# Kernel tuning notes

Measured on AMD Instinct MI355X. Metric: run time of the kernel, lower is better.

The kernel has to match this reference:

```python
import jax, jax.numpy as jnp
import numpy as np

B, T, HIDDEN, QLR = 1, 2560, 7168, 1536
N_HEADS, HEAD_DIM, ROPE_DIM, TOPK = 64, 128, 64, 2048
LN_EPS = 1e-6


def _rope(x, cos, sin):
    # non-interleaved (half-split) rotary: pairs are (x[i], x[i+d/2])
    d = x.shape[-1] // 2
    x1, x2 = x[..., :d], x[..., d:]
    return jnp.concatenate([x1 * cos - x2 * sin, x1 * sin + x2 * cos], axis=-1)


def setup_inputs() -> dict:
    key = jax.random.key(0)
    ks = jax.random.split(key, 6)
    x = jax.random.normal(ks[0], (B, T, HIDDEN), dtype=jnp.float32)
    qr = jax.random.normal(ks[1], (B, T, QLR), dtype=jnp.float32)
    # rope tables (theta = 10000)
    inv_freq = 1.0 / (10000.0 ** (jnp.arange(0, ROPE_DIM, 2, dtype=jnp.float32) / ROPE_DIM))
    angles = jnp.arange(T, dtype=jnp.float32)[:, None] * inv_freq[None, :]  # [T, 32]
    freqs_cos = jnp.cos(angles)
    freqs_sin = jnp.sin(angles)
    # causal additive mask
    i = jnp.arange(T)
    mask = jnp.where(i[None, :, None] >= i[None, None, :], 0.0, -1e9).astype(jnp.float32)  # [1,T,T]
    # params (torch Linear stored transposed so y = x @ W)
    s = 0.02
    wq_b = jax.random.normal(ks[2], (QLR, N_HEADS * HEAD_DIM), dtype=jnp.float32) * s
    wk_w = jax.random.normal(ks[3], (HIDDEN, HEAD_DIM), dtype=jnp.float32) * s
    k_gamma = jnp.ones((HEAD_DIM,), dtype=jnp.float32)
    k_beta = jnp.zeros((HEAD_DIM,), dtype=jnp.float32)
    wproj = jax.random.normal(ks[4], (HIDDEN, N_HEADS), dtype=jnp.float32) * s
    return {"x": x, "qr": qr, "freqs_cos": freqs_cos, "freqs_sin": freqs_sin,
            "mask": mask, "wq_b": wq_b, "wk_w": wk_w, "k_gamma": k_gamma,
            "k_beta": k_beta, "wproj": wproj}


def reference(x, qr, freqs_cos, freqs_sin, mask, wq_b, wk_w, k_gamma, k_beta, wproj):
    bsz, seqlen, _ = x.shape
    # queries
    q = (qr @ wq_b).reshape(bsz, seqlen, N_HEADS, HEAD_DIM)
    q_pe, q_nope = q[..., :ROPE_DIM], q[..., ROPE_DIM:]
    q_pe = _rope(q_pe, freqs_cos[None, :, None, :], freqs_sin[None, :, None, :])
    q = jnp.concatenate([q_pe, q_nope], axis=-1)  # [B,T,H,D]
    # keys: layernorm(wk(x))
    k = x @ wk_w  # [B,T,D]
    mu = jnp.mean(k, axis=-1, keepdims=True)
    var = jnp.mean(jnp.square(k - mu), axis=-1, keepdims=True)
    k = (k - mu) / jnp.sqrt(var + LN_EPS) * k_gamma + k_beta
    k_pe, k_nope = k[..., :ROPE_DIM], k[..., ROPE_DIM:]
    k_pe = _rope(k_pe, freqs_cos[None, :, :], freqs_sin[None, :, :])
    k = jnp.concatenate([k_pe, k_nope], axis=-1)  # [B,S,D]
    # per-head weights
    weights = (x @ wproj) * (N_HEADS ** -0.5) * (HEAD_DIM ** -0.5)  # [B,T,H]
    # relu score + weighted head reduce
    logits = jax.nn.relu(jnp.einsum('bthd,bsd->btsh', q, k))  # [B,T,S,H]
    index_score = jnp.einsum('btsh,bth->bts', logits, weights) + mask
    # top-k + scatter mask
    kk = min(TOPK, seqlen)
    _, topk_idx = jax.lax.top_k(index_score, kk)  # [B,T,K]
    index_mask = jnp.full((bsz, seqlen, seqlen), -1e9, dtype=jnp.float32)
    bi = jnp.arange(bsz)[:, None, None]
    ti = jnp.arange(seqlen)[None, :, None]
    index_mask = index_mask.at[bi, ti, topk_idx].set(0.0)
    return index_mask
```

## Files before the change

### kernel.cpp

```cpp
#include <hip/hip_runtime.h>
#include <cstdint>

#define T_SEQ   2560
#define HID     7168
#define QLRD    1536
#define NHEAD   64
#define HDIM    128
#define TOPK    2048
#define T0SEL   2048
#define NSEL    512

#define QHOFF 0
#define QLOFF 2097152
#define KOFF  4194304
#define WOFF  4521984
#define KHOFF 4554752
#define KLOFF 4718592
#define SOFF  5242880

typedef _Float16 half8 __attribute__((ext_vector_type(8)));
typedef _Float16 half4v __attribute__((ext_vector_type(4)));
typedef float    floatx16 __attribute__((ext_vector_type(16)));

__device__ __forceinline__ void lds_barrier() {
    asm volatile("s_waitcnt lgkmcnt(0)" ::: "memory");
    __builtin_amdgcn_s_barrier();
}

#define SWZ(row) ((((row) >> 3) & 3) << 3)

__global__ __launch_bounds__(384) void kw_kernel(
        const float* __restrict__ x, const float* __restrict__ wk,
        const float* __restrict__ wp, float* __restrict__ Pk,
        float* __restrict__ Pw, long pkstride, long pwstride, int klen) {
    const int t0 = blockIdx.x * 64;
    const int chunk = blockIdx.y;
    const int k0 = chunk * klen;
    const int kl = min(klen, HID - k0);
    const int steps = kl >> 5;
    float* pk = Pk + (size_t)chunk * pkstride;
    float* pw = Pw + (size_t)chunk * pwstride;

    const int tid = threadIdx.x;
    const int lane = tid & 63;
    const int wv = tid >> 6;
    const int wt = wv / 3;
    const int wn2 = wv % 3;
    const int l31 = lane & 31;
    const int kb = (lane >> 5) * 8;

    __shared__ __align__(16) _Float16 Ah0[64 * 40], Al0[64 * 40];
    __shared__ __align__(16) _Float16 Bh0[192 * 40], Bl0[192 * 40];
    __shared__ __align__(16) _Float16 Ah1[64 * 40], Al1[64 * 40];
    __shared__ __align__(16) _Float16 Bh1[192 * 40], Bl1[192 * 40];

    const int am = tid >> 2;
    const int ak = (tid & 3) * 8;
    const int akS = ak ^ SWZ(am);
    const int bkr = (tid / 48) * 4;
    const int bnr = (tid % 48) * 4;

    const float* aB = x + (size_t)(t0 + am) * HID + k0 + ak;
    const float* bsrc; int bld, bcol;
    if (bnr < 128) { bsrc = wk; bld = 128; bcol = bnr; }
    else           { bsrc = wp; bld = 64;  bcol = bnr - 128; }
    const float* bB = bsrc + (size_t)(k0 + bkr) * bld + bcol;

    float4 pa0, pa1, pb0, pb1, pb2, pb3;

#define KWLOAD(KK) do {                                                        \
    const float* ap_ = aB + (size_t)(KK) * 32;                                 \
    const float* bp_ = bB + (size_t)(KK) * 32 * bld;                           \
    if (tid < 256) { pa0 = *(const float4*)(ap_ + 0);                          \
                     pa1 = *(const float4*)(ap_ + 4); }                        \
    pb0 = *(const float4*)(bp_ + 0 * (size_t)bld);                             \
    pb1 = *(const float4*)(bp_ + 1 * (size_t)bld);                             \
    pb2 = *(const float4*)(bp_ + 2 * (size_t)bld);                             \
    pb3 = *(const float4*)(bp_ + 3 * (size_t)bld);                             \
} while (0)

#define KWCONVERT(AH, AL, BH, BL) do {                                         \
    if (tid < 256) {                                                           \
        float av[8];                                                           \
        *(float4*)&av[0] = pa0; *(float4*)&av[4] = pa1;                        \
        half8 ha, la;                                                          \
        _Pragma("unroll")                                                      \
        for (int i = 0; i < 8; ++i) {                                          \
            float v = av[i];                                                   \
            _Float16 hi = (_Float16)v;                                         \
            ha[i] = hi;                                                        \
            la[i] = (_Float16)(v - (float)hi);                                 \
        }                                                                      \
        *(half8*)&AH[am * 40 + akS] = ha;                                      \
        *(half8*)&AL[am * 40 + akS] = la;                                      \
    }                                                                          \
    {                                                                          \
        float bv[4][4];                                                        \
        *(float4*)&bv[0][0] = pb0; *(float4*)&bv[1][0] = pb1;                  \
        *(float4*)&bv[2][0] = pb2; *(float4*)&bv[3][0] = pb3;                  \
        _Pragma("unroll")                                                      \
        for (int j = 0; j < 4; ++j) {                                          \
            const int bkS = bkr ^ SWZ(bnr + j);                                \
            half4v hb, lb;                                                     \
            _Pragma("unroll")                                                  \
            for (int i = 0; i < 4; ++i) {                                      \
                float v = bv[i][j] * 64.0f;                                    \
                _Float16 hi = (_Float16)v;                                     \
                hb[i] = hi;                                                    \
                lb[i] = (_Float16)(v - (float)hi);                             \
            }                                                                  \
            *(half4v*)&BH[(bnr + j) * 40 + bkS] = hb;                          \
            *(half4v*)&BL[(bnr + j) * 40 + bkS] = lb;                          \
        }                                                                      \
    }                                                                          \
} while (0)

    const int rowA  = wt * 32 + l31;
    const int xA    = SWZ(rowA);
    const int rowB0 = wn2 * 64 + l31;
    const int xB0   = SWZ(rowB0);
    const int rowB1 = rowB0 + 32;
    const int xB1   = SWZ(rowB1);

#define KWMFMA(AH, AL, BH, BL) do {                                            \
    __builtin_amdgcn_s_setprio(1);                                             \
    _Pragma("unroll")                                                          \
    for (int c = 0; c < 2; ++c) {                                              \
        const int ka = c * 16 + kb;                                            \
        half8 ah  = *(const half8*)&AH[rowA * 40 + (ka ^ xA)];                 \
        half8 al  = *(const half8*)&AL[rowA * 40 + (ka ^ xA)];                 \
        half8 bh0 = *(const half8*)&BH[rowB0 * 40 + (ka ^ xB0)];               \
        half8 bl0 = *(const half8*)&BL[rowB0 * 40 + (ka ^ xB0)];               \
        half8 bh1 = *(const half8*)&BH[rowB1 * 40 + (ka ^ xB1)];               \
        half8 bl1 = *(const half8*)&BL[rowB1 * 40 + (ka ^ xB1)];               \
        Chh0 = __builtin_amdgcn_mfma_f32_32x32x16_f16(ah, bh0, Chh0, 0, 0, 0); \
        Chl0 = __builtin_amdgcn_mfma_f32_32x32x16_f16(ah, bl0, Chl0, 0, 0, 0); \
        Clh0 = __builtin_amdgcn_mfma_f32_32x32x16_f16(al, bh0, Clh0, 0, 0, 0); \
        Chh1 = __builtin_amdgcn_mfma_f32_32x32x16_f16(ah, bh1, Chh1, 0, 0, 0); \
        Chl1 = __builtin_amdgcn_mfma_f32_32x32x16_f16(ah, bl1, Chl1, 0, 0, 0); \
        Clh1 = __builtin_amdgcn_mfma_f32_32x32x16_f16(al, bh1, Clh1, 0, 0, 0); \
    }                                                                          \
    __builtin_amdgcn_s_setprio(0);                                             \
} while (0)

    floatx16 Z = {0.f,0.f,0.f,0.f,0.f,0.f,0.f,0.f,0.f,0.f,0.f,0.f,0.f,0.f,0.f,0.f};
    floatx16 Chh0 = Z, Chl0 = Z, Clh0 = Z;
    floatx16 Chh1 = Z, Chl1 = Z, Clh1 = Z;

    KWLOAD(0);
    KWCONVERT(Ah0, Al0, Bh0, Bl0);
    KWLOAD(1);
    __builtin_amdgcn_sched_barrier(0);
    lds_barrier();

    for (int ks = 0; ks < steps; ks += 2) {
        KWMFMA(Ah0, Al0, Bh0, Bl0);
        KWCONVERT(Ah1, Al1, Bh1, Bl1);
        KWLOAD(min(ks + 2, steps - 1));
        __builtin_amdgcn_sched_barrier(0);
        lds_barrier();
        KWMFMA(Ah1, Al1, Bh1, Bl1);
        KWCONVERT(Ah0, Al0, Bh0, Bl0);
        KWLOAD(min(ks + 3, steps - 1));
        __builtin_amdgcn_sched_barrier(0);
        lds_barrier();
    }
#undef KWLOAD
#undef KWCONVERT
#undef KWMFMA

    const int rbase = wt * 32 + 4 * (lane >> 5);
#pragma unroll
    for (int r = 0; r < 16; ++r) {
        int trow = t0 + rbase + (r & 3) + 8 * (r >> 2);
        float v0 = ((Chh0[r] + Chl0[r]) + Clh0[r]) * 0.015625f;
        float v1 = ((Chh1[r] + Chl1[r]) + Clh1[r]) * 0.015625f;
        int c0 = wn2 * 64 + l31;
        if (wn2 < 2) {
            pk[(size_t)trow * 128 + c0] = v0;
            pk[(size_t)trow * 128 + c0 + 32] = v1;
        } else if (trow >= T0SEL) {
            pw[(size_t)(trow - T0SEL) * 64 + c0 - 128] = v0;
            pw[(size_t)(trow - T0SEL) * 64 + c0 - 96] = v1;
        }
    }
}

__global__ void reduce2_kernel(float* __restrict__ dk, const float* __restrict__ sk,
                               long kstr, float* __restrict__ dw,
                               const float* __restrict__ sw, long wstr, int nchunk) {
    int i = blockIdx.x * 256 + threadIdx.x;
    if (i < 327680) {
        float s = sk[i];
        for (int c = 1; c < nchunk; ++c) s += sk[(size_t)c * kstr + i];
        dk[i] = s;
    } else {
        int j = i - 327680;
        float s = sw[j];
        for (int c = 1; c < nchunk; ++c) s += sw[(size_t)c * wstr + j];
        dw[j] = s;
    }
}

__global__ void lnrope_kernel(const float* __restrict__ fcos, const float* __restrict__ fsin,
                              const float* __restrict__ gamma, const float* __restrict__ beta,
                              const float* __restrict__ Kbuf, float* __restrict__ Wbuf,
                              _Float16* __restrict__ KhG, _Float16* __restrict__ KlG) {
#pragma clang fp contract(off)
    const int s = blockIdx.x;
    const int d = threadIdx.x;
    __shared__ float red[128];
    __shared__ float kn[128];
    float kv = Kbuf[(size_t)s * 128 + d];
    red[d] = kv;
    __syncthreads();
    for (int off = 64; off > 0; off >>= 1) {
        if (d < off) red[d] += red[d + off];
        __syncthreads();
    }
    float mu = red[0] / 128.0f;
    __syncthreads();
    float dv = kv - mu;
    red[d] = dv * dv;
    __syncthreads();
    for (int off = 64; off > 0; off >>= 1) {
        if (d < off) red[d] += red[d + off];
        __syncthreads();
    }
    float var = red[0] / 128.0f;
    float nrm = dv / sqrtf(var + 1e-6f);
    nrm = nrm * gamma[d] + beta[d];
    kn[d] = nrm;
    __syncthreads();
    float o;
    if (d < 64) {
        int p = d & 31;
        float c = fcos[s * 32 + p], sn = fsin[s * 32 + p];
        if (d < 32) o = kn[d] * c - kn[d + 32] * sn;
        else        o = kn[d - 32] * sn + kn[d] * c;
    } else {
        o = kn[d];
    }
    _Float16 hi = (_Float16)o;
    _Float16 lo = (_Float16)(o - (float)hi);
    KhG[(size_t)s * 128 + d] = hi;
    KlG[(size_t)s * 128 + d] = lo;
    if (s >= T0SEL && d < 64) {
        Wbuf[(size_t)(s - T0SEL) * 64 + d] *= (0.125f * 0.08838834764831845f);
    }
}

__global__ __launch_bounds__(256, 2) void q_kernel(
        const float* __restrict__ qr, const float* __restrict__ wqb,
        const float* __restrict__ fcos, const float* __restrict__ fsin,
        _Float16* __restrict__ QhG, _Float16* __restrict__ QlG) {
    const int head = blockIdx.x;
    const int bx = blockIdx.y;
    const int tid = threadIdx.x;
    const int lane = tid & 63;
    const int wv = tid >> 6;
    const int wt = wv >> 1, wn = wv & 1;
    const int l31 = lane & 31;
    const int kb = (lane >> 5) * 8;

    __shared__ __align__(16) _Float16 Ah0[64 * 40], Al0[64 * 40];
    __shared__ __align__(16) _Float16 Bh0[128 * 40], Bl0[128 * 40];
    __shared__ __align__(16) _Float16 Ah1[64 * 40], Al1[64 * 40];
    __shared__ __align__(16) _Float16 Bh1[128 * 40], Bl1[128 * 40];

    const int am = tid >> 2;
    const int ak = (tid & 3) * 8;
    const int akS = ak ^ SWZ(am);
    const int bn = (tid & 31) * 4;
    const int bk = (tid >> 5) * 4;

    const float* aB = qr + (size_t)(T0SEL + bx * 64 + am) * QLRD + ak;
    const float* bB = wqb + (size_t)bk * 8192 + head * 128 + bn;

    float4 pa0, pa1, pb0, pb1, pb2, pb3;

#define QLOAD(KK) do {                                                         \
    const float* ap_ = aB + (size_t)(KK) * 32;                                 \
    const float* bp_ = bB + (size_t)(KK) * 32 * 8192;                          \
    pa0 = *(const float4*)(ap_ + 0);                                           \
    pa1 = *(const float4*)(ap_ + 4);                                           \
    pb0 = *(const float4*)(bp_ + 0 * 8192);                                    \
    pb1 = *(const float4*)(bp_ + 1 * 8192);                                    \
    pb2 = *(const float4*)(bp_ + 2 * 8192);                                    \
    pb3 = *(const float4*)(bp_ + 3 * 8192);                                    \
} while (0)

#define QCONVERT(AH, AL, BH, BL) do {                                          \
    float av[8];                                                               \
    *(float4*)&av[0] = pa0; *(float4*)&av[4] = pa1;                            \
    half8 ha, la;                                                              \
    _Pragma("unroll")                                                          \
    for (int i = 0; i < 8; ++i) {                                              \
        float v = av[i];                                                       \
        _Float16 hi = (_Float16)v;                                             \
        ha[i] = hi;                                                            \
        la[i] = (_Float16)(v - (float)hi);                                     \
    }                                                                          \
    *(half8*)&AH[am * 40 + akS] = ha;                                          \
    *(half8*)&AL[am * 40 + akS] = la;                                          \
    float bv[4][4];                                                            \
    *(float4*)&bv[0][0] = pb0; *(float4*)&bv[1][0] = pb1;                      \
    *(float4*)&bv[2][0] = pb2; *(float4*)&bv[3][0] = pb3;                      \
    _Pragma("unroll")                                                          \
    for (int j = 0; j < 4; ++j) {                                              \
        const int bkS = bk ^ SWZ(bn + j);                                      \
        half4v hb, lb;                                                         \
        _Pragma("unroll")                                                      \
        for (int i = 0; i < 4; ++i) {                                          \
            float v = bv[i][j] * 64.0f;                                        \
            _Float16 hi = (_Float16)v;                                         \
            hb[i] = hi;                                                        \
            lb[i] = (_Float16)(v - (float)hi);                                 \
        }                                                                      \
        *(half4v*)&BH[(bn + j) * 40 + bkS] = hb;                               \
        *(half4v*)&BL[(bn + j) * 40 + bkS] = lb;                               \
    }                                                                          \
} while (0)

    const int rowA  = wt * 32 + l31;
    const int xA    = SWZ(rowA);
    const int rowB0 = wn * 64 + l31;
    const int xB0   = SWZ(rowB0);
    const int rowB1 = rowB0 + 32;
    const int xB1   = SWZ(rowB1);

#define QMFMA(AH, AL, BH, BL) do {                                             \
    __builtin_amdgcn_s_setprio(1);                                             \
    _Pragma("unroll")                                                          \
    for (int c = 0; c < 2; ++c) {                                              \
        const int ka = c * 16 + kb;                                            \
        half8 ah  = *(const half8*)&AH[rowA * 40 + (ka ^ xA)];                 \
        half8 al  = *(const half8*)&AL[rowA * 40 + (ka ^ xA)];                 \
        half8 bh0 = *(const half8*)&BH[rowB0 * 40 + (ka ^ xB0)];               \
        half8 bl0 = *(const half8*)&BL[rowB0 * 40 + (ka ^ xB0)];               \
        half8 bh1 = *(const half8*)&BH[rowB1 * 40 + (ka ^ xB1)];               \
        half8 bl1 = *(const half8*)&BL[rowB1 * 40 + (ka ^ xB1)];               \
        Chh0 = __builtin_amdgcn_mfma_f32_32x32x16_f16(ah, bh0, Chh0, 0, 0, 0); \
        Chl0 = __builtin_amdgcn_mfma_f32_32x32x16_f16(ah, bl0, Chl0, 0, 0, 0); \
        Clh0 = __builtin_amdgcn_mfma_f32_32x32x16_f16(al, bh0, Clh0, 0, 0, 0); \
        Chh1 = __builtin_amdgcn_mfma_f32_32x32x16_f16(ah, bh1, Chh1, 0, 0, 0); \
        Chl1 = __builtin_amdgcn_mfma_f32_32x32x16_f16(ah, bl1, Chl1, 0, 0, 0); \
        Clh1 = __builtin_amdgcn_mfma_f32_32x32x16_f16(al, bh1, Clh1, 0, 0, 0); \
    }                                                                          \
    __builtin_amdgcn_s_setprio(0);                                             \
} while (0)

    floatx16 Z = {0.f,0.f,0.f,0.f,0.f,0.f,0.f,0.f,0.f,0.f,0.f,0.f,0.f,0.f,0.f,0.f};
    floatx16 Chh0 = Z, Chl0 = Z, Clh0 = Z;
    floatx16 Chh1 = Z, Chl1 = Z, Clh1 = Z;

    const int steps = QLRD / 32;

    QLOAD(0);
    QCONVERT(Ah0, Al0, Bh0, Bl0);
    QLOAD(1);
    __builtin_amdgcn_sched_barrier(0);
    lds_barrier();

    for (int ks = 0; ks < steps; ks += 2) {
        QMFMA(Ah0, Al0, Bh0, Bl0);
        QCONVERT(Ah1, Al1, Bh1, Bl1);
        QLOAD(min(ks + 2, steps - 1));
        __builtin_amdgcn_sched_barrier(0);
        lds_barrier();
        QMFMA(Ah1, Al1, Bh1, Bl1);
        QCONVERT(Ah0, Al0, Bh0, Bl0);
        QLOAD(min(ks + 3, steps - 1));
        __builtin_amdgcn_sched_barrier(0);
        lds_barrier();
    }
#undef QLOAD
#undef QCONVERT
#undef QMFMA

    {
#pragma clang fp contract(off)
        const int tbase = bx * 64 + wt * 32 + 4 * (lane >> 5);
#pragma unroll
        for (int r = 0; r < 16; ++r) {
            int tl = tbase + (r & 3) + 8 * (r >> 2);
            float v0 = ((Chh0[r] + Chl0[r]) + Clh0[r]) * 0.015625f;
            float v1 = ((Chh1[r] + Chl1[r]) + Clh1[r]) * 0.015625f;
            float o0, o1;
            if (wn == 0) {
                int tg = T0SEL + tl;
                float c = fcos[tg * 32 + l31];
                float s = fsin[tg * 32 + l31];
                o0 = v0 * c - v1 * s;
                o1 = v0 * s + v1 * c;
            } else {
                o0 = v0; o1 = v1;
            }
            int d0 = wn * 64 + l31;
            size_t off = (size_t)head * 65536 + (size_t)tl * 128;
            _Float16 h0 = (_Float16)o0;
            _Float16 h1 = (_Float16)o1;
            QhG[off + d0] = h0;
            QlG[off + d0] = (_Float16)(o0 - (float)h0);
            QhG[off + d0 + 32] = h1;
            QlG[off + d0 + 32] = (_Float16)(o1 - (float)h1);
        }
    }
}

__global__ __launch_bounds__(256) void score_kernel(
        const _Float16* __restrict__ Qh, const _Float16* __restrict__ Ql,
        const _Float16* __restrict__ Kh, const _Float16* __restrict__ Kl,
        const float* __restrict__ Wbuf, float* __restrict__ S0,
        float* __restrict__ S1, int hcnt) {
    const int bid = blockIdx.x;
    const int tt0 = (bid & 15) * 32;
    const int s0  = (bid >> 4) * 128;
    const int hb  = blockIdx.y * hcnt;
    float* __restrict__ dst = blockIdx.y ? S1 : S0;
    const int tid = threadIdx.x;
    const int wv  = tid >> 6;
    const int lane = tid & 63;
    const int l31 = lane & 31;
    const int kb  = (lane >> 5) * 8;

    __shared__ __align__(16) _Float16 AhA[32 * 136];
    __shared__ __align__(16) _Float16 AlA[32 * 136];
    __shared__ __align__(16) _Float16 AhB[32 * 136];
    __shared__ __align__(16) _Float16 AlB[32 * 136];
    __shared__ float WsT[64 * 36];

    half8 Bh[8], Bl[8];
    {
        const int srow = s0 + wv * 32 + l31;
        const _Float16* kh = Kh + (size_t)srow * 128 + kb;
        const _Float16* kl = Kl + (size_t)srow * 128 + kb;
#pragma unroll
        for (int c = 0; c < 8; ++c) {
            Bh[c] = *(const half8*)(kh + c * 16);
            Bl[c] = *(const half8*)(kl + c * 16);
        }
    }
#pragma unroll
    for (int r = 0; r < 8; ++r) {
        int idx = tid + 256 * r;
        int row = idx >> 6, h = idx & 63;
        WsT[h * 36 + row] = Wbuf[(size_t)(tt0 + row) * 64 + h];
    }

    const int srow0 = tid >> 4;
    const int scc0  = (tid & 15) * 8;
    const int srow1 = srow0 + 16;
    const int scc1  = scc0;

    const _Float16* qhp = Qh + (size_t)hb * 65536 + (size_t)tt0 * 128;
    const _Float16* qlp = Ql + (size_t)hb * 65536 + (size_t)tt0 * 128;

    half8 sh0 = *(const half8*)&qhp[srow0 * 128 + scc0];
    half8 sh1 = *(const half8*)&qhp[srow1 * 128 + scc1];
    half8 sl0 = *(const half8*)&qlp[srow0 * 128 + scc0];
    half8 sl1 = *(const half8*)&qlp[srow1 * 128 + scc1];
    *(half8*)&AhA[srow0 * 136 + scc0] = sh0;
    *(half8*)&AhA[srow1 * 136 + scc1] = sh1;
    *(half8*)&AlA[srow0 * 136 + scc0] = sl0;
    *(half8*)&AlA[srow1 * 136 + scc1] = sl1;
    qhp += 65536; qlp += 65536;
    sh0 = *(const half8*)&qhp[srow0 * 128 + scc0];
    sh1 = *(const half8*)&qhp[srow1 * 128 + scc1];
    sl0 = *(const half8*)&qlp[srow0 * 128 + scc0];
    sl1 = *(const half8*)&qlp[srow1 * 128 + scc1];
    __builtin_amdgcn_sched_barrier(0);
    lds_barrier();

    float S[16];
#pragma unroll
    for (int r = 0; r < 16; ++r) S[r] = 0.0f;

#define SCORE_COMPUTE(AH, AL, HIDX)                                            \
    {                                                                          \
        floatx16 C0 = {0.f,0.f,0.f,0.f,0.f,0.f,0.f,0.f,                        \
                       0.f,0.f,0.f,0.f,0.f,0.f,0.f,0.f};                       \
        floatx16 C2 = C0, C3 = C0;                                             \
        __builtin_amdgcn_s_setprio(1);                                         \
        _Pragma("unroll")                                                      \
        for (int c = 0; c < 8; ++c) {                                          \
            half8 a_h = *(const half8*)&AH[l31 * 136 + c * 16 + kb];           \
            half8 a_l = *(const half8*)&AL[l31 * 136 + c * 16 + kb];           \
            C0 = __builtin_amdgcn_mfma_f32_32x32x16_f16(a_h, Bh[c], C0, 0, 0, 0); \
            C2 = __builtin_amdgcn_mfma_f32_32x32x16_f16(a_h, Bl[c], C2, 0, 0, 0); \
            C3 = __builtin_amdgcn_mfma_f32_32x32x16_f16(a_l, Bh[c], C3, 0, 0, 0); \
        }                                                                      \
        __builtin_amdgcn_s_setprio(0);                                         \
        const float* wb = &WsT[(HIDX) * 36 + 4 * (lane >> 5)];                 \
        float4 w0 = *(const float4*)(wb + 0);                                  \
        float4 w1 = *(const float4*)(wb + 8);                                  \
        float4 w2 = *(const float4*)(wb + 16);                                 \
        float4 w3 = *(const float4*)(wb + 24);                                 \
        float w[16] = {w0.x, w0.y, w0.z, w0.w, w1.x, w1.y, w1.z, w1.w,         \
                       w2.x, w2.y, w2.z, w2.w, w3.x, w3.y, w3.z, w3.w};        \
        _Pragma("unroll")                                                      \
        for (int r = 0; r < 16; ++r) {                                         \
            float L = (C0[r] + C2[r]) + C3[r];                                 \
            S[r] += w[r] * fmaxf(L, 0.0f);                                     \
        }                                                                      \
    }

    for (int h = 0; h < hcnt; h += 2) {
        SCORE_COMPUTE(AhA, AlA, hb + h)
        *(half8*)&AhB[srow0 * 136 + scc0] = sh0;
        *(half8*)&AhB[srow1 * 136 + scc1] = sh1;
        *(half8*)&AlB[srow0 * 136 + scc0] = sl0;
        *(half8*)&AlB[srow1 * 136 + scc1] = sl1;
        qhp += 65536; qlp += 65536;
        sh0 = *(const half8*)&qhp[srow0 * 128 + scc0];
        sh1 = *(const half8*)&qhp[srow1 * 128 + scc1];
        sl0 = *(const half8*)&qlp[srow0 * 128 + scc0];
        sl1 = *(const half8*)&qlp[srow1 * 128 + scc1];
        __builtin_amdgcn_sched_barrier(0);
        lds_barrier();

        SCORE_COMPUTE(AhB, AlB, hb + h + 1)
        *(half8*)&AhA[srow0 * 136 + scc0] = sh0;
        *(half8*)&AhA[srow1 * 136 + scc1] = sh1;
        *(half8*)&AlA[srow0 * 136 + scc0] = sl0;
        *(half8*)&AlA[srow1 * 136 + scc1] = sl1;
        qhp += 65536; qlp += 65536;
        sh0 = *(const half8*)&qhp[srow0 * 128 + scc0];
        sh1 = *(const half8*)&qhp[srow1 * 128 + scc1];
        sl0 = *(const half8*)&qlp[srow0 * 128 + scc0];
        sl1 = *(const half8*)&qlp[srow1 * 128 + scc1];
        __builtin_amdgcn_sched_barrier(0);
        lds_barrier();
    }
#undef SCORE_COMPUTE

    const int scol = s0 + wv * 32 + l31;
#pragma unroll
    for (int r = 0; r < 16; ++r) {
        int trow = tt0 + (r & 3) + 8 * (r >> 2) + 4 * (lane >> 5);
        dst[(size_t)trow * 2560 + scol] = S[r] + 0.0f;
    }
}

__global__ void finalize_kernel(float* __restrict__ out, const float* __restrict__ S1) {
    const int row_id = blockIdx.x;
    const int tid = threadIdx.x;

    if (row_id < T0SEL) {
        const float4 zero4 = make_float4(0.0f, 0.0f, 0.0f, 0.0f);
        const float4 neg4 = make_float4(-1000000000.0f, -1000000000.0f,
                                        -1000000000.0f, -1000000000.0f);
        for (int i = tid; i < T_SEQ / 4; i += 256) {
            *(float4*)&out[(size_t)row_id * T_SEQ + i * 4] = (i * 4 < TOPK) ? zero4 : neg4;
        }
        return;
    }

    const int t = row_id;
    const int n = t + 1;
    float* row = out + (size_t)t * T_SEQ;
    const float* s1p = S1 ? (S1 + (size_t)(t - T0SEL) * T_SEQ) : nullptr;

    __shared__ unsigned U[T_SEQ];
    __shared__ int hist[256];
    __shared__ int aux[256];
    __shared__ unsigned sh_prefix;
    __shared__ int sh_kneed;

    for (int i = tid; i < T_SEQ; i += 256) {
        unsigned u = 0u;
        if (i < n) {
            float sc = row[i];
            if (s1p) sc += s1p[i];
            int b = __float_as_int(sc);
            u = (b < 0) ? ~((unsigned)b) : (((unsigned)b) | 0x80000000u);
        }
        U[i] = u;
    }
    if (tid == 0) { sh_prefix = 0u; sh_kneed = TOPK; }
    __syncthreads();

    for (int pass = 0; pass < 4; ++pass) {
        const int shift = 24 - 8 * pass;
        const unsigned himask = (pass == 0) ? 0u : (0xFFFFFFFFu << (shift + 8));
        hist[tid] = 0;
        __syncthreads();
        const unsigned pre = sh_prefix;
        const int kneed = sh_kneed;
        for (int i = tid; i < T_SEQ; i += 256) {
            unsigned u = U[i];
            if ((u & himask) == pre) atomicAdd(&hist[(u >> shift) & 255], 1);
        }
        __syncthreads();
        aux[tid] = hist[tid];
        __syncthreads();
        for (int off = 1; off < 256; off <<= 1) {
            int a = (tid + off < 256) ? aux[tid + off] : 0;
            __syncthreads();
            aux[tid] += a;
            __syncthreads();
        }
        int above = (tid < 255) ? aux[tid + 1] : 0;
        if (above < kneed && kneed <= aux[tid]) {
            sh_prefix = pre | (((unsigned)tid) << shift);
            sh_kneed = kneed - above;
        }
        __syncthreads();
    }
    const unsigned theta = sh_prefix;
    const int r = sh_kneed;

    const int s_lo = tid * 10, s_hi = s_lo + 10;
    int c = 0;
    for (int s = s_lo; s < s_hi; ++s) c += (U[s] == theta);
    aux[tid] = c;
    __syncthreads();
    for (int off = 1; off < 256; off <<= 1) {
        int a = (tid >= off) ? aux[tid - off] : 0;
        __syncthreads();
        aux[tid] += a;
        __syncthreads();
    }
    int rank = aux[tid] - c;
    for (int s = s_lo; s < s_hi; ++s) {
        unsigned u = U[s];
        bool sel = (u > theta) || (u == theta && rank < r);
        if (u == theta) ++rank;
        row[s] = sel ? 0.0f : -1000000000.0f;
    }
}

extern "C" void kernel_launch(void* const* d_in, const int* in_sizes, int n_in,
                              void* d_out, int out_size, void* d_ws, size_t ws_size,
                              hipStream_t stream) {
    (void)in_sizes; (void)n_in; (void)out_size;
    const float* x     = (const float*)d_in[0];
    const float* qr    = (const float*)d_in[1];
    const float* fcos  = (const float*)d_in[2];
    const float* fsin  = (const float*)d_in[3];
    const float* wqb   = (const float*)d_in[5];
    const float* wk    = (const float*)d_in[6];
    const float* gamma = (const float*)d_in[7];
    const float* beta  = (const float*)d_in[8];
    const float* wp    = (const float*)d_in[9];

    float* out  = (float*)d_out;
    float* Kbuf = out + KOFF;
    float* Wbuf = out + WOFF;
    float* Sbuf = out + SOFF;
    _Float16* QhG = (_Float16*)(out + QHOFF);
    _Float16* QlG = (_Float16*)(out + QLOFF);
    _Float16* KhG = (_Float16*)(out + KHOFF);
    _Float16* KlG = (_Float16*)(out + KLOFF);

    const size_t need = (size_t)(6 * 327680 + 6 * 32768) * 4;
    int nchunk; int klen; float *Pk, *Pw; long pkstride, pwstride;
    if (ws_size >= need) {
        nchunk = 6; klen = 1216;
        Pk = (float*)d_ws;            pkstride = 327680;
        Pw = (float*)d_ws + 1966080;  pwstride = 32768;
    } else {
        nchunk = 2; klen = 3584;
        Pk = out + KOFF;  pkstride = 360448;
        Pw = out + WOFF;  pwstride = 360448;
    }

    const size_t s1_need = (size_t)NSEL * T_SEQ * sizeof(float);
    float* S1 = (ws_size >= s1_need) ? (float*)d_ws : nullptr;

    kw_kernel<<<dim3(40, nchunk), 384, 0, stream>>>(x, wk, wp, Pk, Pw, pkstride, pwstride, klen);
    reduce2_kernel<<<1408, 256, 0, stream>>>(Kbuf, Pk, pkstride, Wbuf, Pw, pwstride, nchunk);
    lnrope_kernel<<<T_SEQ, 128, 0, stream>>>(fcos, fsin, gamma, beta, Kbuf, Wbuf, KhG, KlG);
    q_kernel<<<dim3(64, 8), 256, 0, stream>>>(qr, wqb, fcos, fsin, QhG, QlG);
    if (S1) {
        score_kernel<<<dim3(320, 2), 256, 0, stream>>>(QhG, QlG, KhG, KlG, Wbuf, Sbuf, S1, 32);
    } else {
        score_kernel<<<dim3(320, 1), 256, 0, stream>>>(QhG, QlG, KhG, KlG, Wbuf, Sbuf, nullptr, 64);
    }
    finalize_kernel<<<T_SEQ, 256, 0, stream>>>(out, S1);
}
```

Before: 362.7 us.

## Process two heads per barrier stage and overlap epilogue with next MFMA

New measurement: 433.7 us. 19.6% more time.

```diff
diff --git a/kernel.cpp b/kernel.cpp
--- a/kernel.cpp
+++ b/kernel.cpp
@@ -408,7 +408,7 @@
     }
 }
 
-__global__ __launch_bounds__(256) void score_kernel(
+__global__ __launch_bounds__(256, 2) void score_kernel(
         const _Float16* __restrict__ Qh, const _Float16* __restrict__ Ql,
         const _Float16* __restrict__ Kh, const _Float16* __restrict__ Kl,
         const float* __restrict__ Wbuf, float* __restrict__ S0,
@@ -424,10 +424,10 @@
     const int l31 = lane & 31;
     const int kb  = (lane >> 5) * 8;
 
-    __shared__ __align__(16) _Float16 AhA[32 * 136];
-    __shared__ __align__(16) _Float16 AlA[32 * 136];
-    __shared__ __align__(16) _Float16 AhB[32 * 136];
-    __shared__ __align__(16) _Float16 AlB[32 * 136];
+    __shared__ __align__(16) _Float16 PhE[32 * 136], PlE[32 * 136];
+    __shared__ __align__(16) _Float16 PhO[32 * 136], PlO[32 * 136];
+    __shared__ __align__(16) _Float16 RhE[32 * 136], RlE[32 * 136];
+    __shared__ __align__(16) _Float16 RhO[32 * 136], RlO[32 * 136];
     __shared__ float WsT[64 * 36];
 
     half8 Bh[8], Bl[8];
@@ -451,24 +451,34 @@
     const int srow0 = tid >> 4;
     const int scc0  = (tid & 15) * 8;
     const int srow1 = srow0 + 16;
-    const int scc1  = scc0;
 
     const _Float16* qhp = Qh + (size_t)hb * 65536 + (size_t)tt0 * 128;
     const _Float16* qlp = Ql + (size_t)hb * 65536 + (size_t)tt0 * 128;
 
-    half8 sh0 = *(const half8*)&qhp[srow0 * 128 + scc0];
-    half8 sh1 = *(const half8*)&qhp[srow1 * 128 + scc1];
-    half8 sl0 = *(const half8*)&qlp[srow0 * 128 + scc0];
-    half8 sl1 = *(const half8*)&qlp[srow1 * 128 + scc1];
-    *(half8*)&AhA[srow0 * 136 + scc0] = sh0;
-    *(half8*)&AhA[srow1 * 136 + scc1] = sh1;
-    *(half8*)&AlA[srow0 * 136 + scc0] = sl0;
-    *(half8*)&AlA[srow1 * 136 + scc1] = sl1;
-    qhp += 65536; qlp += 65536;
-    sh0 = *(const half8*)&qhp[srow0 * 128 + scc0];
-    sh1 = *(const half8*)&qhp[srow1 * 128 + scc1];
-    sl0 = *(const half8*)&qlp[srow0 * 128 + scc0];
-    sl1 = *(const half8*)&qlp[srow1 * 128 + scc1];
+    half8 sEh0, sEh1, sEl0, sEl1;
+    half8 sOh0, sOh1, sOl0, sOl1;
+
+#define SLOAD(RH0, RH1, RL0, RL1) do {                                         \
+    RH0 = *(const half8*)&qhp[srow0 * 128 + scc0];                             \
+    RH1 = *(const half8*)&qhp[srow1 * 128 + scc0];                             \
+    RL0 = *(const half8*)&qlp[srow0 * 128 + scc0];                             \
+    RL1 = *(const half8*)&qlp[srow1 * 128 + scc0];                             \
+    qhp += 65536; qlp += 65536;                                                \
+} while (0)
+
+#define SWRITE(DH, DL, RH0, RH1, RL0, RL1) do {                                \
+    *(half8*)&DH[srow0 * 136 + scc0] = RH0;                                    \
+    *(half8*)&DH[srow1 * 136 + scc0] = RH1;                                    \
+    *(half8*)&DL[srow0 * 136 + scc0] = RL0;                                    \
+    *(half8*)&DL[srow1 * 136 + scc0] = RL1;                                    \
+} while (0)
+
+    SLOAD(sEh0, sEh1, sEl0, sEl1);
+    SWRITE(PhE, PlE, sEh0, sEh1, sEl0, sEl1);
+    SLOAD(sOh0, sOh1, sOl0, sOl1);
+    SWRITE(PhO, PlO, sOh0, sOh1, sOl0, sOl1);
+    SLOAD(sEh0, sEh1, sEl0, sEl1);
+    SLOAD(sOh0, sOh1, sOl0, sOl1);
     __builtin_amdgcn_sched_barrier(0);
     lds_barrier();
 
@@ -476,63 +486,70 @@
 #pragma unroll
     for (int r = 0; r < 16; ++r) S[r] = 0.0f;
 
-#define SCORE_COMPUTE(AH, AL, HIDX)                                            \
-    {                                                                          \
-        floatx16 C0 = {0.f,0.f,0.f,0.f,0.f,0.f,0.f,0.f,                        \
-                       0.f,0.f,0.f,0.f,0.f,0.f,0.f,0.f};                       \
-        floatx16 C2 = C0, C3 = C0;                                             \
-        __builtin_amdgcn_s_setprio(1);                                         \
-        _Pragma("unroll")                                                      \
-        for (int c = 0; c < 8; ++c) {                                          \
-            half8 a_h = *(const half8*)&AH[l31 * 136 + c * 16 + kb];           \
-            half8 a_l = *(const half8*)&AL[l31 * 136 + c * 16 + kb];           \
-            C0 = __builtin_amdgcn_mfma_f32_32x32x16_f16(a_h, Bh[c], C0, 0, 0, 0); \
-            C2 = __builtin_amdgcn_mfma_f32_32x32x16_f16(a_h, Bl[c], C2, 0, 0, 0); \
-            C3 = __builtin_amdgcn_mfma_f32_32x32x16_f16(a_l, Bh[c], C3, 0, 0, 0); \
-        }                                                                      \
-        __builtin_amdgcn_s_setprio(0);                                         \
-        const float* wb = &WsT[(HIDX) * 36 + 4 * (lane >> 5)];                 \
-        float4 w0 = *(const float4*)(wb + 0);                                  \
-        float4 w1 = *(const float4*)(wb + 8);                                  \
-        float4 w2 = *(const float4*)(wb + 16);                                 \
-        float4 w3 = *(const float4*)(wb + 24);                                 \
-        float w[16] = {w0.x, w0.y, w0.z, w0.w, w1.x, w1.y, w1.z, w1.w,         \
-                       w2.x, w2.y, w2.z, w2.w, w3.x, w3.y, w3.z, w3.w};        \
-        _Pragma("unroll")                                                      \
-        for (int r = 0; r < 16; ++r) {                                         \
-            float L = (C0[r] + C2[r]) + C3[r];                                 \
-            S[r] += w[r] * fmaxf(L, 0.0f);                                     \
-        }                                                                      \
-    }
-
-    for (int h = 0; h < hcnt; h += 2) {
-        SCORE_COMPUTE(AhA, AlA, hb + h)
-        *(half8*)&AhB[srow0 * 136 + scc0] = sh0;
-        *(half8*)&AhB[srow1 * 136 + scc1] = sh1;
-        *(half8*)&AlB[srow0 * 136 + scc0] = sl0;
-        *(half8*)&AlB[srow1 * 136 + scc1] = sl1;
-        qhp += 65536; qlp += 65536;
-        sh0 = *(const half8*)&qhp[srow0 * 128 + scc0];
-        sh1 = *(const half8*)&qhp[srow1 * 128 + scc1];
-        sl0 = *(const half8*)&qlp[srow0 * 128 + scc0];
-        sl1 = *(const half8*)&qlp[srow1 * 128 + scc1];
-        __builtin_amdgcn_sched_barrier(0);
-        lds_barrier();
-
-        SCORE_COMPUTE(AhB, AlB, hb + h + 1)
-        *(half8*)&AhA[srow0 * 136 + scc0] = sh0;
-        *(half8*)&AhA[srow1 * 136 + scc1] = sh1;
-        *(half8*)&AlA[srow0 * 136 + scc0] = sl0;
-        *(half8*)&AlA[srow1 * 136 + scc1] = sl1;
-        qhp += 65536; qlp += 65536;
-        sh0 = *(const half8*)&qhp[srow0 * 128 + scc0];
-        sh1 = *(const half8*)&qhp[srow1 * 128 + scc1];
-        sl0 = *(const half8*)&qlp[srow0 * 128 + scc0];
-        sl1 = *(const half8*)&qlp[srow1 * 128 + scc1];
-        __builtin_amdgcn_sched_barrier(0);
-        lds_barrier();
-    }
-#undef SCORE_COMPUTE
+#define SMFMA(AH, AL, CC0, CC2, CC3) do {                                      \
+    __builtin_amdgcn_s_setprio(1);                                             \
+    _Pragma("unroll")                                                          \
+    for (int c = 0; c < 8; ++c) {                                              \
+        half8 a_h = *(const half8*)&AH[l31 * 136 + c * 16 + kb];               \
+        half8 a_l = *(const half8*)&AL[l31 * 136 + c * 16 + kb];               \
+        CC0 = __builtin_amdgcn_mfma_f32_32x32x16_f16(a_h, Bh[c], CC0, 0, 0, 0);\
+        CC2 = __builtin_amdgcn_mfma_f32_32x32x16_f16(a_h, Bl[c], CC2, 0, 0, 0);\
+        CC3 = __builtin_amdgcn_mfma_f32_32x32x16_f16(a_l, Bh[c], CC3, 0, 0, 0);\
+    }                                                                          \
+    __builtin_amdgcn_s_setprio(0);                                             \
+} while (0)
+
+#define SEPI(CC0, CC2, CC3, HIDX) do {                                         \
+    const float* wb = &WsT[(HIDX) * 36 + 4 * (lane >> 5)];                     \
+    float4 w0 = *(const float4*)(wb + 0);                                      \
+    float4 w1 = *(const float4*)(wb + 8);                                      \
+    float4 w2 = *(const float4*)(wb + 16);                                     \
+    float4 w3 = *(const float4*)(wb + 24);                                     \
+    float w[16] = {w0.x, w0.y, w0.z, w0.w, w1.x, w1.y, w1.z, w1.w,             \
+                   w2.x, w2.y, w2.z, w2.w, w3.x, w3.y, w3.z, w3.w};            \
+    _Pragma("unroll")                                                          \
+    for (int r = 0; r < 16; ++r) {                                             \
+        float L = (CC0[r] + CC2[r]) + CC3[r];                                  \
+        S[r] += w[r] * fmaxf(L, 0.0f);                                         \
+    }                                                                          \
+} while (0)
+
+    const floatx16 Z = {0.f,0.f,0.f,0.f,0.f,0.f,0.f,0.f,0.f,0.f,0.f,0.f,0.f,0.f,0.f,0.f};
+
+    for (int p = 0; p < hcnt; p += 4) {
+        {
+            floatx16 C0e = Z, C2e = Z, C3e = Z;
+            floatx16 C0o = Z, C2o = Z, C3o = Z;
+            SMFMA(PhE, PlE, C0e, C2e, C3e);
+            SMFMA(PhO, PlO, C0o, C2o, C3o);
+            SWRITE(RhE, RlE, sEh0, sEh1, sEl0, sEl1);
+            SWRITE(RhO, RlO, sOh0, sOh1, sOl0, sOl1);
+            SLOAD(sEh0, sEh1, sEl0, sEl1);
+            SLOAD(sOh0, sOh1, sOl0, sOl1);
+            __builtin_amdgcn_sched_barrier(0);
+            lds_barrier();
+            SEPI(C0e, C2e, C3e, hb + p);
+            SEPI(C0o, C2o, C3o, hb + p + 1);
+        }
+        {
+            floatx16 C0e = Z, C2e = Z, C3e = Z;
+            floatx16 C0o = Z, C2o = Z, C3o = Z;
+            SMFMA(RhE, RlE, C0e, C2e, C3e);
+            SMFMA(RhO, RlO, C0o, C2o, C3o);
+            SWRITE(PhE, PlE, sEh0, sEh1, sEl0, sEl1);
+            SWRITE(PhO, PlO, sOh0, sOh1, sOl0, sOl1);
+            SLOAD(sEh0, sEh1, sEl0, sEl1);
+            SLOAD(sOh0, sOh1, sOl0, sOl1);
+            __builtin_amdgcn_sched_barrier(0);
+            lds_barrier();
+            SEPI(C0e, C2e, C3e, hb + p + 2);
+            SEPI(C0o, C2o, C3o, hb + p + 3);
+        }
+    }
+#undef SLOAD
+#undef SWRITE
+#undef SMFMA
+#undef SEPI
 
     const int scol = s0 + wv * 32 + l31;
 #pragma unroll
```
